# Kernel tuning notes

Measured on AMD Instinct MI355X. Metric: run time of the kernel, lower is better.

The kernel has to match this reference:

```python
import jax, jax.numpy as jnp
import numpy as np
from jax import lax


def quick_gelu(x):
    return x * jax.nn.sigmoid(1.702 * x)


def setup_inputs() -> dict:
    key = jax.random.key(0)
    ks = jax.random.split(key, 12)
    B, H, W, C, D, M = 32, 56, 56, 192, 64, 8
    g = lambda k, shape, s: (jax.random.normal(k, shape, jnp.float32) * s)
    return {
        "x": jax.random.normal(ks[0], (B, H, W, C), jnp.float32),
        "W1": g(ks[1], (64, C), 0.05),
        "b1": jnp.zeros((64,), jnp.float32),
        "W2": g(ks[2], (64, 64), 0.05),
        "b2": jnp.zeros((64,), jnp.float32),
        "mask_token": g(ks[3], (M, 64), 0.05),
        "Wh": g(ks[4], (D * D * 9, 64), 0.02),
        "bh": g(ks[5], (D * D * 9,), 0.02),
        "Wd": g(ks[6], (D, C), 0.05),
        "bd": jnp.zeros((D,), jnp.float32),
        "Wu": g(ks[7], (C, D), 0.02),
        "bu": jnp.zeros((C,), jnp.float32),
    }


def reference(x, W1, b1, W2, b2, mask_token, Wh, bh, Wd, bd, Wu, bu):
    B, H, W_, C = x.shape
    D = Wd.shape[0]
    M = mask_token.shape[0]
    # meta_net: Linear -> ReLU -> Linear, [B,H,W,64]
    pf = jax.nn.relu(jnp.einsum("bhwc,kc->bhwk", x, W1) + b1)
    pf = jnp.einsum("bhwk,jk->bhwj", pf, W2) + b2
    # mask routing: [M,B,H,W], softmax over spatial positions
    mask = jnp.einsum("bhwk,mk->mbhw", pf, mask_token)
    mask = jax.nn.softmax(mask.reshape(M, B, -1), axis=-1).reshape(M, B, H, W_)
    # sum_m mask[m][...,None]*pf, then sum over H,W -> [B,64]
    mwf = (mask.sum(0)[..., None] * pf).sum(axis=(1, 2))
    # hypernet: per-sample conv weights [B,D,D,3,3]
    conv_w = (jnp.einsum("bk,ok->bo", mwf, Wh) + bh).reshape(B, D, D, 3, 3)
    # adapter_down + QuickGELU, [B,D,H,W]
    xd = jnp.einsum("bhwc,dc->bhwd", x, Wd) + bd
    xp = quick_gelu(xd.transpose(0, 3, 1, 2))

    def conv1(xi, wi):  # xi [D,H,W], wi [D,D,3,3]
        return lax.conv_general_dilated(xi[None], wi, (1, 1), [(1, 1), (1, 1)])[0]

    xc = jax.vmap(conv1)(xp, conv_w)  # [B,D,H,W]
    xd2 = quick_gelu(xc.transpose(0, 2, 3, 1))  # [B,H,W,D]
    # dropout(p=0.1) is identity in eval mode
    xu = jnp.einsum("bhwd,cd->bhwc", xd2, Wu) + bu
    return xu + x
```

## Files before the change

### kernel.cpp

```cpp
#include <hip/hip_runtime.h>

typedef unsigned short ushort_t;
typedef short bf16x8 __attribute__((ext_vector_type(8)));
typedef float f32x4 __attribute__((ext_vector_type(4)));

#define MFMA(a, b, c) __builtin_amdgcn_mfma_f32_16x16x32_bf16(a, b, c, 0, 0, 0)

#define B_    32
#define HW_   3136
#define NPOS  100352

__device__ __forceinline__ float bf2f(unsigned short h) {
    return __uint_as_float(((unsigned int)h) << 16);
}
__device__ __forceinline__ unsigned short f2bf(float f) {
    unsigned int u = __float_as_uint(f);
    u += 0x7FFFu + ((u >> 16) & 1u);
    return (unsigned short)(u >> 16);
}
__device__ __forceinline__ float qgelu(float v) {
    return v / (1.0f + __expf(-1.702f * v));
}
__device__ __forceinline__ void unpack8(uint4 v, float* f) {
    f[0] = bf2f((unsigned short)(v.x & 0xffff)); f[1] = bf2f((unsigned short)(v.x >> 16));
    f[2] = bf2f((unsigned short)(v.y & 0xffff)); f[3] = bf2f((unsigned short)(v.y >> 16));
    f[4] = bf2f((unsigned short)(v.z & 0xffff)); f[5] = bf2f((unsigned short)(v.z >> 16));
    f[6] = bf2f((unsigned short)(v.w & 0xffff)); f[7] = bf2f((unsigned short)(v.w >> 16));
}

__global__ __launch_bounds__(256) void k0_prep(
    const float* __restrict__ W1, const float* __restrict__ W2,
    const float* __restrict__ mtok, const float* __restrict__ Wd,
    const float* __restrict__ Wu,
    ushort_t* __restrict__ w1f, ushort_t* __restrict__ wdf,
    ushort_t* __restrict__ w2f, ushort_t* __restrict__ mtf,
    ushort_t* __restrict__ wuf)
{
    const int gid = blockIdx.x * 256 + threadIdx.x;
    const int stride = gridDim.x * 256;
    for (int i = gid; i < 12288; i += stride) {
        int j = i & 7, lane = (i >> 3) & 63, nt = (i >> 9) & 3, kc = i >> 11;
        int n = nt * 16 + (lane & 15), k = kc * 32 + (lane >> 4) * 8 + j;
        w1f[i] = f2bf(W1[n * 192 + k]);
        wdf[i] = f2bf(Wd[n * 192 + k]);
    }
    for (int i = gid; i < 4096; i += stride) {
        int j = i & 7, lane = (i >> 3) & 63, nt = (i >> 9) & 3, kc = i >> 11;
        int n = nt * 16 + (lane & 15), k = kc * 32 + (lane >> 4) * 8 + j;
        w2f[i] = f2bf(W2[n * 64 + k]);
    }
    for (int i = gid; i < 1024; i += stride) {
        int j = i & 7, lane = (i >> 3) & 63, kc = i >> 9;
        int n = lane & 15, k = kc * 32 + (lane >> 4) * 8 + j;
        mtf[i] = (n < 8) ? f2bf(mtok[n * 64 + k]) : (ushort_t)0;
    }
    for (int i = gid; i < 12288; i += stride) {
        int j = i & 7, lane = (i >> 3) & 63, g = i >> 9;
        int nt = g % 12, kc = g / 12;
        int n = nt * 16 + (lane & 15), k = kc * 32 + (lane >> 4) * 8 + j;
        wuf[i] = f2bf(Wu[n * 64 + k]);
    }
}

__global__ __launch_bounds__(256) void k1_meta_adapter(
    const float* __restrict__ x, const float* __restrict__ b1,
    const float* __restrict__ b2, const float* __restrict__ bd,
    const ushort_t* __restrict__ w1f, const ushort_t* __restrict__ wdf,
    const ushort_t* __restrict__ w2f, const ushort_t* __restrict__ mtf,
    ushort_t* __restrict__ pf2g, ushort_t* __restrict__ xpg,
    float* __restrict__ Lg)
{
    __shared__ ushort_t xs[64 * 200];
    __shared__ ushort_t pf1s[4][16 * 72];

    const int tid = threadIdx.x;
    const int posBase = blockIdx.x * 64;

    #pragma unroll
    for (int t = 0; t < 6; t++) {
        int u = tid + t * 256;
        int pos = u / 24, c8 = u % 24;
        const float4* gp = (const float4*)(x + ((size_t)(posBase + pos)) * 192 + c8 * 8);
        float4 v0 = gp[0], v1 = gp[1];
        bf16x8 r;
        r[0] = (short)f2bf(v0.x); r[1] = (short)f2bf(v0.y);
        r[2] = (short)f2bf(v0.z); r[3] = (short)f2bf(v0.w);
        r[4] = (short)f2bf(v1.x); r[5] = (short)f2bf(v1.y);
        r[6] = (short)f2bf(v1.z); r[7] = (short)f2bf(v1.w);
        *(bf16x8*)&xs[pos * 200 + c8 * 8] = r;
    }
    __syncthreads();

    const int lane = tid & 63, wv = tid >> 6;
    const int col = lane & 15, q = lane >> 4;

    bf16x8 A[6];
    #pragma unroll
    for (int kc = 0; kc < 6; kc++)
        A[kc] = *(const bf16x8*)&xs[(wv * 16 + col) * 200 + kc * 32 + q * 8];

    f32x4 acc1[4], acc3[4];
    #pragma unroll
    for (int nt = 0; nt < 4; nt++) { acc1[nt] = (f32x4)0.0f; acc3[nt] = (f32x4)0.0f; }

    #pragma unroll
    for (int kc = 0; kc < 6; kc++) {
        #pragma unroll
        for (int nt = 0; nt < 4; nt++) {
            bf16x8 B1 = *(const bf16x8*)(w1f + ((kc * 4 + nt) * 64 + lane) * 8);
            acc1[nt] = MFMA(A[kc], B1, acc1[nt]);
            bf16x8 Bd = *(const bf16x8*)(wdf + ((kc * 4 + nt) * 64 + lane) * 8);
            acc3[nt] = MFMA(A[kc], Bd, acc3[nt]);
        }
    }
    __syncthreads();

    #pragma unroll
    for (int nt = 0; nt < 4; nt++) {
        float bias = b1[nt * 16 + col];
        #pragma unroll
        for (int r = 0; r < 4; r++) {
            float v = acc1[nt][r] + bias;
            v = v > 0.0f ? v : 0.0f;
            pf1s[wv][(q * 4 + r) * 72 + nt * 16 + col] = f2bf(v);
        }
    }

    f32x4 acc2[4];
    #pragma unroll
    for (int nt = 0; nt < 4; nt++) acc2[nt] = (f32x4)0.0f;
    #pragma unroll
    for (int kc = 0; kc < 2; kc++) {
        bf16x8 A2 = *(const bf16x8*)&pf1s[wv][col * 72 + kc * 32 + q * 8];
        #pragma unroll
        for (int nt = 0; nt < 4; nt++) {
            bf16x8 B2 = *(const bf16x8*)(w2f + ((kc * 4 + nt) * 64 + lane) * 8);
            acc2[nt] = MFMA(A2, B2, acc2[nt]);
        }
    }

    #pragma unroll
    for (int nt = 0; nt < 4; nt++) {
        float bias = bd[nt * 16 + col];
        #pragma unroll
        for (int r = 0; r < 4; r++) {
            float v = qgelu(acc3[nt][r] + bias);
            xs[(wv * 16 + q * 4 + r) * 72 + nt * 16 + col] = f2bf(v);
        }
    }

    #pragma unroll
    for (int nt = 0; nt < 4; nt++) {
        float bias = b2[nt * 16 + col];
        #pragma unroll
        for (int r = 0; r < 4; r++)
            pf1s[wv][(q * 4 + r) * 72 + nt * 16 + col] = f2bf(acc2[nt][r] + bias);
    }

    f32x4 Lacc = (f32x4)0.0f;
    #pragma unroll
    for (int kc = 0; kc < 2; kc++) {
        bf16x8 A3 = *(const bf16x8*)&pf1s[wv][col * 72 + kc * 32 + q * 8];
        bf16x8 Bm = *(const bf16x8*)(mtf + (kc * 64 + lane) * 8);
        Lacc = MFMA(A3, Bm, Lacc);
    }
    if (col < 8) {
        #pragma unroll
        for (int r = 0; r < 4; r++)
            Lg[((size_t)(posBase + wv * 16 + q * 4 + r)) * 8 + col] = Lacc[r];
    }
    __syncthreads();

    #pragma unroll
    for (int t = 0; t < 2; t++) {
        int u = tid + t * 256;
        int pos = u >> 3, c8 = u & 7;
        uint4 vx = *(const uint4*)&xs[pos * 72 + c8 * 8];
        *(uint4*)(xpg + ((size_t)(posBase + pos)) * 64 + c8 * 8) = vx;
        uint4 vp = *(const uint4*)&pf1s[pos >> 4][(pos & 15) * 72 + c8 * 8];
        *(uint4*)(pf2g + ((size_t)(posBase + pos)) * 64 + c8 * 8) = vp;
    }
}

__global__ __launch_bounds__(256) void k2_mask_mwf(
    const float* __restrict__ Lg, const ushort_t* __restrict__ pf2g,
    float* __restrict__ mwfg)
{
    __shared__ float masksum[HW_];
    __shared__ float wred[4][8];
    __shared__ float smx[8];
    __shared__ float sinv[8];
    __shared__ float sred[32 * 64];

    const int tid = threadIdx.x;
    const int b = blockIdx.x;
    const int lane = tid & 63, wv = tid >> 6;
    const float* Lb = Lg + (size_t)b * HW_ * 8;

    float lmax[8];
    #pragma unroll
    for (int m = 0; m < 8; m++) lmax[m] = -1e30f;
    for (int p = tid; p < HW_; p += 256) {
        const float4* lp = (const float4*)(Lb + (size_t)p * 8);
        float4 a = lp[0], c = lp[1];
        lmax[0] = fmaxf(lmax[0], a.x); lmax[1] = fmaxf(lmax[1], a.y);
        lmax[2] = fmaxf(lmax[2], a.z); lmax[3] = fmaxf(lmax[3], a.w);
        lmax[4] = fmaxf(lmax[4], c.x); lmax[5] = fmaxf(lmax[5], c.y);
        lmax[6] = fmaxf(lmax[6], c.z); lmax[7] = fmaxf(lmax[7], c.w);
    }
    #pragma unroll
    for (int m = 0; m < 8; m++) {
        float v = lmax[m];
        for (int off = 32; off > 0; off >>= 1) v = fmaxf(v, __shfl_down(v, off));
        lmax[m] = v;
    }
    if (lane == 0) {
        #pragma unroll
        for (int m = 0; m < 8; m++) wred[wv][m] = lmax[m];
    }
    __syncthreads();
    if (tid < 8)
        smx[tid] = fmaxf(fmaxf(wred[0][tid], wred[1][tid]), fmaxf(wred[2][tid], wred[3][tid]));
    __syncthreads();

    float lsum[8];
    #pragma unroll
    for (int m = 0; m < 8; m++) lsum[m] = 0.0f;
    for (int p = tid; p < HW_; p += 256) {
        const float4* lp = (const float4*)(Lb + (size_t)p * 8);
        float4 a = lp[0], c = lp[1];
        lsum[0] += __expf(a.x - smx[0]); lsum[1] += __expf(a.y - smx[1]);
        lsum[2] += __expf(a.z - smx[2]); lsum[3] += __expf(a.w - smx[3]);
        lsum[4] += __expf(c.x - smx[4]); lsum[5] += __expf(c.y - smx[5]);
        lsum[6] += __expf(c.z - smx[6]); lsum[7] += __expf(c.w - smx[7]);
    }
    #pragma unroll
    for (int m = 0; m < 8; m++) {
        float v = lsum[m];
        for (int off = 32; off > 0; off >>= 1) v += __shfl_down(v, off);
        lsum[m] = v;
    }
    __syncthreads();
    if (lane == 0) {
        #pragma unroll
        for (int m = 0; m < 8; m++) wred[wv][m] = lsum[m];
    }
    __syncthreads();
    if (tid < 8)
        sinv[tid] = 1.0f / (wred[0][tid] + wred[1][tid] + wred[2][tid] + wred[3][tid]);
    __syncthreads();

    for (int p = tid; p < HW_; p += 256) {
        const float4* lp = (const float4*)(Lb + (size_t)p * 8);
        float4 a = lp[0], c = lp[1];
        float ms = __expf(a.x - smx[0]) * sinv[0] + __expf(a.y - smx[1]) * sinv[1]
                 + __expf(a.z - smx[2]) * sinv[2] + __expf(a.w - smx[3]) * sinv[3]
                 + __expf(c.x - smx[4]) * sinv[4] + __expf(c.y - smx[5]) * sinv[5]
                 + __expf(c.z - smx[6]) * sinv[6] + __expf(c.w - smx[7]) * sinv[7];
        masksum[p] = ms;
    }
    __syncthreads();

    const int part = tid >> 3, kg = tid & 7;
    float a8[8];
    #pragma unroll
    for (int j = 0; j < 8; j++) a8[j] = 0.0f;
    for (int p = part; p < HW_; p += 32) {
        float ms = masksum[p];
        uint4 v = *(const uint4*)(pf2g + ((size_t)b * HW_ + p) * 64 + kg * 8);
        float f[8]; unpack8(v, f);
        #pragma unroll
        for (int j = 0; j < 8; j++) a8[j] += ms * f[j];
    }
    #pragma unroll
    for (int j = 0; j < 8; j++) sred[part * 64 + kg * 8 + j] = a8[j];
    __syncthreads();
    if (tid < 64) {
        float s = 0.0f;
        #pragma unroll
        for (int pt = 0; pt < 32; pt++) s += sred[pt * 64 + tid];
        mwfg[b * 64 + tid] = s;
    }
}

__global__ __launch_bounds__(256) void k3_hypernet(
    const float* __restrict__ mwfg, const float* __restrict__ Whg,
    const float* __restrict__ bhg, ushort_t* __restrict__ cwb)
{
    __shared__ float mwfs[32 * 64];
    const int tid = threadIdx.x;
    for (int i = tid; i < 2048; i += 256) mwfs[i] = mwfg[i];
    __syncthreads();

    const int op = blockIdx.x * 256 + tid;
    const int j = op & 7, lane = (op >> 3) & 63, nt = (op >> 9) & 3;
    const int kc = (op >> 11) & 1, tap = op >> 12;
    const int oc = nt * 16 + (lane & 15);
    const int ic = kc * 32 + (lane >> 4) * 8 + j;
    const int o = oc * 576 + ic * 9 + tap;

    float wreg[64];
    const float4* src = (const float4*)(Whg + (size_t)o * 64);
    #pragma unroll
    for (int t = 0; t < 16; t++) {
        float4 v = src[t];
        wreg[t * 4 + 0] = v.x; wreg[t * 4 + 1] = v.y;
        wreg[t * 4 + 2] = v.z; wreg[t * 4 + 3] = v.w;
    }
    const float bias = bhg[o];
    for (int b = 0; b < 32; b++) {
        float a = bias;
        #pragma unroll
        for (int k = 0; k < 64; k++) a += mwfs[b * 64 + k] * wreg[k];
        cwb[(size_t)b * 36864 + op] = f2bf(a);
    }
}

__global__ __launch_bounds__(128) void k4_conv(
    const ushort_t* __restrict__ xpg, const ushort_t* __restrict__ cwb,
    ushort_t* __restrict__ xd2g)
{
    __shared__ ushort_t xs[2 * 348 * 40];

    const int tid = threadIdx.x;
    const int b = blockIdx.x / 14, yt = blockIdx.x % 14, y0 = yt * 4;

    for (int u = tid; u < 2784; u += 128) {
        int r = u / 464, rem = u % 464, c = rem >> 3, c8 = rem & 7;
        int gy = y0 - 1 + r, gx = c - 1;
        uint4 v = make_uint4(0, 0, 0, 0);
        if (gy >= 0 && gy < 56 && gx >= 0 && gx < 56)
            v = *(const uint4*)(xpg + ((size_t)b * HW_ + gy * 56 + gx) * 64 + c8 * 8);
        int kc = c8 >> 2, q = c8 & 3;
        *(uint4*)&xs[kc * 13920 + (r * 58 + c) * 40 + q * 8] = v;
    }
    __syncthreads();

    const int lane = tid & 63, wv = tid >> 6;
    const int col = lane & 15, q = lane >> 4;

    int abase[7];
    #pragma unroll
    for (int t = 0; t < 7; t++) {
        int p = (wv * 7 + t) * 16 + col;
        int row = p / 56, cc = p - row * 56;
        abase[t] = ((row * 58 + cc) * 40 + q * 8) * 2;
    }

    f32x4 acc[7][4];
    #pragma unroll
    for (int t = 0; t < 7; t++)
        #pragma unroll
        for (int nt = 0; nt < 4; nt++) acc[t][nt] = (f32x4)0.0f;

    const ushort_t* wbase = cwb + (size_t)b * 36864;
    for (int tap = 0; tap < 9; tap++) {
        const int dy = tap / 3, dx = tap % 3;
        const int toff = (dy * 58 + dx) * 80;
        bf16x8 Bf[2][4];
        #pragma unroll
        for (int kc = 0; kc < 2; kc++)
            #pragma unroll
            for (int nt = 0; nt < 4; nt++)
                Bf[kc][nt] = *(const bf16x8*)(wbase + tap * 4096 + ((kc * 4 + nt) * 64 + lane) * 8);
        #pragma unroll
        for (int t = 0; t < 7; t++) {
            bf16x8 A0 = *(const bf16x8*)((const char*)xs + abase[t] + toff);
            bf16x8 A1 = *(const bf16x8*)((const char*)xs + 27840 + abase[t] + toff);
            #pragma unroll
            for (int nt = 0; nt < 4; nt++) {
                acc[t][nt] = MFMA(A0, Bf[0][nt], acc[t][nt]);
                acc[t][nt] = MFMA(A1, Bf[1][nt], acc[t][nt]);
            }
        }
    }
    __syncthreads();

    #pragma unroll
    for (int t = 0; t < 7; t++) {
        int mt = wv * 7 + t;
        #pragma unroll
        for (int nt = 0; nt < 4; nt++)
            #pragma unroll
            for (int r = 0; r < 4; r++)
                xs[(mt * 16 + q * 4 + r) * 72 + nt * 16 + col] = f2bf(qgelu(acc[t][nt][r]));
    }
    __syncthreads();

    for (int u = tid; u < 1792; u += 128) {
        int pos = u >> 3, c8 = u & 7;
        uint4 v = *(const uint4*)&xs[pos * 72 + c8 * 8];
        size_t gpos = (size_t)b * HW_ + (size_t)y0 * 56 + pos;
        *(uint4*)(xd2g + gpos * 64 + c8 * 8) = v;
    }
}

__global__ __launch_bounds__(256) void k5_up_res(
    const ushort_t* __restrict__ xd2g, const ushort_t* __restrict__ wuf,
    const float* __restrict__ bu, const float* __restrict__ xg,
    float* __restrict__ outg)
{
    __shared__ ushort_t xds[64 * 72];

    const int tid = threadIdx.x;
    const size_t posBase = (size_t)blockIdx.x * 64;

    #pragma unroll
    for (int t = 0; t < 2; t++) {
        int u = tid + t * 256;
        int pos = u >> 3, c8 = u & 7;
        uint4 v = *(const uint4*)(xd2g + (posBase + pos) * 64 + c8 * 8);
        *(uint4*)&xds[pos * 72 + c8 * 8] = v;
    }
    __syncthreads();

    const int lane = tid & 63, wv = tid >> 6;
    const int col = lane & 15, q = lane >> 4;

    bf16x8 A[2];
    #pragma unroll
    for (int kc = 0; kc < 2; kc++)
        A[kc] = *(const bf16x8*)&xds[(wv * 16 + col) * 72 + kc * 32 + q * 8];

    f32x4 acc[12];
    #pragma unroll
    for (int nt = 0; nt < 12; nt++) acc[nt] = (f32x4)0.0f;
    #pragma unroll
    for (int kc = 0; kc < 2; kc++)
        #pragma unroll
        for (int nt = 0; nt < 12; nt++) {
            bf16x8 B = *(const bf16x8*)(wuf + ((kc * 12 + nt) * 64 + lane) * 8);
            acc[nt] = MFMA(A[kc], B, acc[nt]);
        }

    #pragma unroll
    for (int nt = 0; nt < 12; nt++) {
        float bias = bu[nt * 16 + col];
        #pragma unroll
        for (int r = 0; r < 4; r++) {
            size_t off = (posBase + wv * 16 + q * 4 + r) * 192 + nt * 16 + col;
            outg[off] = acc[nt][r] + bias + xg[off];
        }
    }
}

extern "C" void kernel_launch(void* const* d_in, const int* in_sizes, int n_in,
                              void* d_out, int out_size, void* d_ws, size_t ws_size,
                              hipStream_t stream) {
    const float* x    = (const float*)d_in[0];
    const float* W1   = (const float*)d_in[1];
    const float* b1   = (const float*)d_in[2];
    const float* W2   = (const float*)d_in[3];
    const float* b2   = (const float*)d_in[4];
    const float* mtok = (const float*)d_in[5];
    const float* Wh   = (const float*)d_in[6];
    const float* bh   = (const float*)d_in[7];
    const float* Wd   = (const float*)d_in[8];
    const float* bd   = (const float*)d_in[9];
    const float* Wu   = (const float*)d_in[10];
    const float* bu   = (const float*)d_in[11];
    float* out = (float*)d_out;

    char* ws = (char*)d_ws;
    ushort_t* pf2 = (ushort_t*)ws;
    ushort_t* xp  = (ushort_t*)(ws + 12845056);
    ushort_t* xd2 = pf2;
    ushort_t* cwb = (ushort_t*)(ws + 25690112);
    float*    mwf = (float*)(ws + 28049408);
    float*    Lg  = (float*)(ws + 28057600);
    ushort_t* w1f = (ushort_t*)(ws + 31268864);
    ushort_t* wdf = (ushort_t*)(ws + 31293440);
    ushort_t* w2f = (ushort_t*)(ws + 31318016);
    ushort_t* mtf = (ushort_t*)(ws + 31326208);
    ushort_t* wuf = (ushort_t*)(ws + 31328256);

    k0_prep<<<48, 256, 0, stream>>>(W1, W2, mtok, Wd, Wu, w1f, wdf, w2f, mtf, wuf);
    k1_meta_adapter<<<1568, 256, 0, stream>>>(x, b1, b2, bd, w1f, wdf, w2f, mtf,
                                              pf2, xp, Lg);
    k2_mask_mwf<<<32, 256, 0, stream>>>(Lg, pf2, mwf);
    k3_hypernet<<<144, 256, 0, stream>>>(mwf, Wh, bh, cwb);
    k4_conv<<<448, 128, 0, stream>>>(xp, cwb, xd2);
    k5_up_res<<<1568, 256, 0, stream>>>(xd2, wuf, bu, x, out);
}
```

Baseline: 272.7 us.

## Split conv into 2-row tiles with waves owning output-channel slices

The per-sample 3x3 conv kernel now processes 2 output rows per block instead of 4, uses 256 threads with each of 4 waves computing one 16-channel output slice across all 112 positions, and launches 896 blocks with a blockIdx swizzle. This cuts the accumulator registers per thread (7 vs 28 MFMA tiles) and the shared memory per block, targeting higher occupancy and more parallelism on the conv stage. In exchange, halo rows are reloaded more often (4 rows loaded per 2 output rows) and A fragments are read redundantly by every wave.

```diff
diff --git a/kernel.cpp b/kernel.cpp
--- a/kernel.cpp
+++ b/kernel.cpp
@@ -316,23 +316,25 @@
     }
 }
 
-__global__ __launch_bounds__(128) void k4_conv(
+__global__ __launch_bounds__(256, 4) void k4_conv(
     const ushort_t* __restrict__ xpg, const ushort_t* __restrict__ cwb,
     ushort_t* __restrict__ xd2g)
 {
-    __shared__ ushort_t xs[2 * 348 * 40];
+    __shared__ ushort_t xs[2 * 232 * 40];
 
     const int tid = threadIdx.x;
-    const int b = blockIdx.x / 14, yt = blockIdx.x % 14, y0 = yt * 4;
-
-    for (int u = tid; u < 2784; u += 128) {
+    const int bid = blockIdx.x;
+    const int swz = (bid & 7) * 112 + (bid >> 3);
+    const int b = swz / 28, yt = swz % 28, y0 = yt * 2;
+
+    for (int u = tid; u < 1856; u += 256) {
         int r = u / 464, rem = u % 464, c = rem >> 3, c8 = rem & 7;
         int gy = y0 - 1 + r, gx = c - 1;
         uint4 v = make_uint4(0, 0, 0, 0);
         if (gy >= 0 && gy < 56 && gx >= 0 && gx < 56)
             v = *(const uint4*)(xpg + ((size_t)b * HW_ + gy * 56 + gx) * 64 + c8 * 8);
         int kc = c8 >> 2, q = c8 & 3;
-        *(uint4*)&xs[kc * 13920 + (r * 58 + c) * 40 + q * 8] = v;
+        *(uint4*)&xs[kc * 9280 + (r * 58 + c) * 40 + q * 8] = v;
     }
     __syncthreads();
 
@@ -342,52 +344,40 @@
     int abase[7];
     #pragma unroll
     for (int t = 0; t < 7; t++) {
-        int p = (wv * 7 + t) * 16 + col;
+        int p = t * 16 + col;
         int row = p / 56, cc = p - row * 56;
         abase[t] = ((row * 58 + cc) * 40 + q * 8) * 2;
     }
 
-    f32x4 acc[7][4];
-    #pragma unroll
-    for (int t = 0; t < 7; t++)
-        #pragma unroll
-        for (int nt = 0; nt < 4; nt++) acc[t][nt] = (f32x4)0.0f;
+    f32x4 acc[7];
+    #pragma unroll
+    for (int t = 0; t < 7; t++) acc[t] = (f32x4)0.0f;
 
     const ushort_t* wbase = cwb + (size_t)b * 36864;
+    #pragma unroll
     for (int tap = 0; tap < 9; tap++) {
         const int dy = tap / 3, dx = tap % 3;
         const int toff = (dy * 58 + dx) * 80;
-        bf16x8 Bf[2][4];
-        #pragma unroll
-        for (int kc = 0; kc < 2; kc++)
-            #pragma unroll
-            for (int nt = 0; nt < 4; nt++)
-                Bf[kc][nt] = *(const bf16x8*)(wbase + tap * 4096 + ((kc * 4 + nt) * 64 + lane) * 8);
+        bf16x8 Bf0 = *(const bf16x8*)(wbase + tap * 4096 + ((0 * 4 + wv) * 64 + lane) * 8);
+        bf16x8 Bf1 = *(const bf16x8*)(wbase + tap * 4096 + ((1 * 4 + wv) * 64 + lane) * 8);
         #pragma unroll
         for (int t = 0; t < 7; t++) {
             bf16x8 A0 = *(const bf16x8*)((const char*)xs + abase[t] + toff);
-            bf16x8 A1 = *(const bf16x8*)((const char*)xs + 27840 + abase[t] + toff);
-            #pragma unroll
-            for (int nt = 0; nt < 4; nt++) {
-                acc[t][nt] = MFMA(A0, Bf[0][nt], acc[t][nt]);
-                acc[t][nt] = MFMA(A1, Bf[1][nt], acc[t][nt]);
-            }
-        }
-    }
-    __syncthreads();
-
-    #pragma unroll
-    for (int t = 0; t < 7; t++) {
-        int mt = wv * 7 + t;
-        #pragma unroll
-        for (int nt = 0; nt < 4; nt++)
-            #pragma unroll
-            for (int r = 0; r < 4; r++)
-                xs[(mt * 16 + q * 4 + r) * 72 + nt * 16 + col] = f2bf(qgelu(acc[t][nt][r]));
-    }
-    __syncthreads();
-
-    for (int u = tid; u < 1792; u += 128) {
+            bf16x8 A1 = *(const bf16x8*)((const char*)xs + 18560 + abase[t] + toff);
+            acc[t] = MFMA(A0, Bf0, acc[t]);
+            acc[t] = MFMA(A1, Bf1, acc[t]);
+        }
+    }
+    __syncthreads();
+
+    #pragma unroll
+    for (int t = 0; t < 7; t++)
+        #pragma unroll
+        for (int r = 0; r < 4; r++)
+            xs[(t * 16 + q * 4 + r) * 72 + wv * 16 + col] = f2bf(qgelu(acc[t][r]));
+    __syncthreads();
+
+    for (int u = tid; u < 896; u += 256) {
         int pos = u >> 3, c8 = u & 7;
         uint4 v = *(const uint4*)&xs[pos * 72 + c8 * 8];
         size_t gpos = (size_t)b * HW_ + (size_t)y0 * 56 + pos;
@@ -479,6 +469,6 @@
                                               pf2, xp, Lg);
     k2_mask_mwf<<<32, 256, 0, stream>>>(Lg, pf2, mwf);
     k3_hypernet<<<144, 256, 0, stream>>>(mwf, Wh, bh, cwb);
-    k4_conv<<<448, 128, 0, stream>>>(xp, cwb, xd2);
+    k4_conv<<<896, 256, 0, stream>>>(xp, cwb, xd2);
     k5_up_res<<<1568, 256, 0, stream>>>(xd2, wuf, bu, x, out);
 }
```

Result: no change. 269.4 us (-1.2%).
